# Kernel tuning notes

Hardware: AMD Instinct MI355X
Metric: run time of the kernel (lower is better)

The kernel has to match this reference:

```python
import jax, jax.numpy as jnp
import numpy as np

B, SEQ, DIM = 8, 4096, 64
THETA = 10000.0


def _make_freqs(seq, dim, theta=THETA):
    # matches torch.polar(ones, outer(t, 1/theta^(2i/dim))) stored as (cos, sin)
    inv = 1.0 / theta ** (np.arange(0, dim, 2, dtype=np.float32) / dim)
    t = np.arange(seq, dtype=np.float32)
    ang = np.outer(t, inv)  # (seq, dim//2)
    return jnp.stack([jnp.cos(ang), jnp.sin(ang)], axis=-1).astype(jnp.float32)  # (seq, dim//2, 2)


def _rope(x, freq):
    # x: (B, S, D); freq: (S, D//2, 2) holding (cos, sin) of the complex freq
    xr = x.reshape(*x.shape[:-1], -1, 2)  # (B, S, D//2, 2)
    a, b = xr[..., 0], xr[..., 1]
    c, s = freq[..., 0], freq[..., 1]
    # complex multiply (a + ib)(c + is)
    out = jnp.stack([a * c - b * s, a * s + b * c], axis=-1)
    return out.reshape(x.shape)


def setup_inputs() -> dict:
    key = jax.random.key(0)
    kq, kk, kv = jax.random.split(key, 3)
    q = jax.random.normal(kq, (B, SEQ, DIM), dtype=jnp.float32)
    k = jax.random.normal(kk, (B, SEQ, DIM), dtype=jnp.float32)
    v = jax.random.normal(kv, (B, SEQ, DIM), dtype=jnp.float32)
    f = _make_freqs(SEQ, DIM)
    return {"q": q, "k": k, "v": v, "freq_q": f, "freq_k": f, "freq_v": f}


def reference(q, k, v, freq_q, freq_k, freq_v):
    q_r = _rope(q, freq_q)
    k_r = _rope(k, freq_k)
    v_r = _rope(v, freq_v)
    scale = jnp.asarray(1.0 / np.sqrt(DIM), dtype=q.dtype)
    scores = jnp.einsum("bqd,bkd->bqk", q_r, k_r) * scale  # unnormalized logits (no softmax)
    return jnp.einsum("bqk,bkd->bqd", scores, v_r)
```

## Files before the change

kernel.cpp:

```cpp
#include <hip/hip_runtime.h>

#define B_ 8
#define S_ 4096
#define D_ 64

__global__ __launch_bounds__(256, 4) void rope_ktv_partials(
    const float* __restrict__ K, const float* __restrict__ V,
    const float* __restrict__ FK, const float* __restrict__ FV,
    float* __restrict__ part, int nchunk, int rowsPerChunk)
{
    __shared__ float kbuf[32][64];
    __shared__ float vbuf[32][64];
    const int t  = threadIdx.x;
    const int b  = blockIdx.x / nchunk;
    const int sBase = (blockIdx.x - b * nchunk) * rowsPerChunk;

    const int sl = t >> 4;
    const int e0 = (t & 15) << 2;
    const int i0 = (t >> 4) << 2;
    const int j0 = (t & 15) << 2;

    const float* kb = K + (size_t)b * S_ * D_;
    const float* vb = V + (size_t)b * S_ * D_;

    float acc[4][4];
    #pragma unroll
    for (int a = 0; a < 4; ++a)
        #pragma unroll
        for (int c = 0; c < 4; ++c) acc[a][c] = 0.f;

    const int nStages = rowsPerChunk >> 5;

    int s = sBase + sl;
    float4 kA = *(const float4*)(kb + (size_t)s * D_ + e0);
    float4 vA = *(const float4*)(vb + (size_t)s * D_ + e0);
    float4 fA = *(const float4*)(FK + (size_t)s * D_ + e0);
    float4 gA = *(const float4*)(FV + (size_t)s * D_ + e0);
    float4 kB = *(const float4*)(kb + (size_t)(s + 16) * D_ + e0);
    float4 vB = *(const float4*)(vb + (size_t)(s + 16) * D_ + e0);
    float4 fB = *(const float4*)(FK + (size_t)(s + 16) * D_ + e0);
    float4 gB = *(const float4*)(FV + (size_t)(s + 16) * D_ + e0);

    for (int it = 0; it < nStages; ++it) {
        float4 kr, vr, kr2, vr2;
        kr.x  = kA.x*fA.x - kA.y*fA.y;  kr.y  = kA.x*fA.y + kA.y*fA.x;
        kr.z  = kA.z*fA.z - kA.w*fA.w;  kr.w  = kA.z*fA.w + kA.w*fA.z;
        vr.x  = vA.x*gA.x - vA.y*gA.y;  vr.y  = vA.x*gA.y + vA.y*gA.x;
        vr.z  = vA.z*gA.z - vA.w*gA.w;  vr.w  = vA.z*gA.w + vA.w*gA.z;
        kr2.x = kB.x*fB.x - kB.y*fB.y;  kr2.y = kB.x*fB.y + kB.y*fB.x;
        kr2.z = kB.z*fB.z - kB.w*fB.w;  kr2.w = kB.z*fB.w + kB.w*fB.z;
        vr2.x = vB.x*gB.x - vB.y*gB.y;  vr2.y = vB.x*gB.y + vB.y*gB.x;
        vr2.z = vB.z*gB.z - vB.w*gB.w;  vr2.w = vB.z*gB.w + vB.w*gB.z;

        if (it > 0) __syncthreads();
        *(float4*)&kbuf[sl][e0]      = kr;
        *(float4*)&vbuf[sl][e0]      = vr;
        *(float4*)&kbuf[sl + 16][e0] = kr2;
        *(float4*)&vbuf[sl + 16][e0] = vr2;
        __syncthreads();

        if (it + 1 < nStages) {
            s = sBase + ((it + 1) << 5) + sl;
            kA = *(const float4*)(kb + (size_t)s * D_ + e0);
            vA = *(const float4*)(vb + (size_t)s * D_ + e0);
            fA = *(const float4*)(FK + (size_t)s * D_ + e0);
            gA = *(const float4*)(FV + (size_t)s * D_ + e0);
            kB = *(const float4*)(kb + (size_t)(s + 16) * D_ + e0);
            vB = *(const float4*)(vb + (size_t)(s + 16) * D_ + e0);
            fB = *(const float4*)(FK + (size_t)(s + 16) * D_ + e0);
            gB = *(const float4*)(FV + (size_t)(s + 16) * D_ + e0);
        }

        #pragma unroll
        for (int r = 0; r < 32; ++r) {
            float4 ka = *(const float4*)&kbuf[r][i0];
            float4 vv = *(const float4*)&vbuf[r][j0];
            acc[0][0] += ka.x*vv.x; acc[0][1] += ka.x*vv.y; acc[0][2] += ka.x*vv.z; acc[0][3] += ka.x*vv.w;
            acc[1][0] += ka.y*vv.x; acc[1][1] += ka.y*vv.y; acc[1][2] += ka.y*vv.z; acc[1][3] += ka.y*vv.w;
            acc[2][0] += ka.z*vv.x; acc[2][1] += ka.z*vv.y; acc[2][2] += ka.z*vv.z; acc[2][3] += ka.z*vv.w;
            acc[3][0] += ka.w*vv.x; acc[3][1] += ka.w*vv.y; acc[3][2] += ka.w*vv.z; acc[3][3] += ka.w*vv.w;
        }
    }

    float* p = part + (size_t)blockIdx.x * (D_ * D_);
    #pragma unroll
    for (int a = 0; a < 4; ++a)
        *(float4*)(p + (size_t)(i0 + a) * D_ + j0) =
            make_float4(acc[a][0], acc[a][1], acc[a][2], acc[a][3]);
}

__global__ __launch_bounds__(256) void reduce_partials(
    const float* __restrict__ part, float* __restrict__ M, int nchunk)
{
    const int g    = blockIdx.x * 256 + threadIdx.x;
    const int b    = g >> 12;
    const int cell = g & 4095;
    const float* p = part + ((size_t)b * nchunk) * (D_ * D_) + cell;
    float s0 = 0.f, s1 = 0.f, s2 = 0.f, s3 = 0.f;
    int i = 0;
    #pragma unroll 8
    for (; i + 4 <= nchunk; i += 4) {
        s0 += p[(size_t)(i + 0) * (D_ * D_)];
        s1 += p[(size_t)(i + 1) * (D_ * D_)];
        s2 += p[(size_t)(i + 2) * (D_ * D_)];
        s3 += p[(size_t)(i + 3) * (D_ * D_)];
    }
    for (; i < nchunk; ++i) s0 += p[(size_t)i * (D_ * D_)];
    M[g] = 0.125f * ((s0 + s1) + (s2 + s3));
}

__global__ __launch_bounds__(256) void rope_q_matmul(
    const float* __restrict__ Q, const float* __restrict__ FQ,
    const float* __restrict__ M, float* __restrict__ OUT, int nb2)
{
    __shared__ float Mt[64][65];
    __shared__ float qbuf[32][64];
    const int t = threadIdx.x;
    const int b = blockIdx.x / nb2;
    const int rowBase = (blockIdx.x - b * nb2) * 32;

    const int sl = t >> 4;
    const int e0 = (t & 15) << 2;
    const float* qb = Q + (size_t)b * S_ * D_;

    const int r1 = rowBase + sl;
    float4 qA = *(const float4*)(qb + (size_t)r1 * D_ + e0);
    float4 fA = *(const float4*)(FQ + (size_t)r1 * D_ + e0);
    float4 qB = *(const float4*)(qb + (size_t)(r1 + 16) * D_ + e0);
    float4 fB = *(const float4*)(FQ + (size_t)(r1 + 16) * D_ + e0);

    const float* mb = M + (size_t)b * (D_ * D_);
    float4 m0 = *(const float4*)(mb + (t << 2));
    float4 m1 = *(const float4*)(mb + 1024 + (t << 2));
    float4 m2 = *(const float4*)(mb + 2048 + (t << 2));
    float4 m3 = *(const float4*)(mb + 3072 + (t << 2));

    float4 qr, qr2;
    qr.x  = qA.x*fA.x - qA.y*fA.y;  qr.y  = qA.x*fA.y + qA.y*fA.x;
    qr.z  = qA.z*fA.z - qA.w*fA.w;  qr.w  = qA.z*fA.w + qA.w*fA.z;
    qr2.x = qB.x*fB.x - qB.y*fB.y;  qr2.y = qB.x*fB.y + qB.y*fB.x;
    qr2.z = qB.z*fB.z - qB.w*fB.w;  qr2.w = qB.z*fB.w + qB.w*fB.z;
    *(float4*)&qbuf[sl][e0]      = qr;
    *(float4*)&qbuf[sl + 16][e0] = qr2;

    {
        const int c0 = (t << 2);
        const float mv[16] = { m0.x, m0.y, m0.z, m0.w,  m1.x, m1.y, m1.z, m1.w,
                               m2.x, m2.y, m2.z, m2.w,  m3.x, m3.y, m3.z, m3.w };
        #pragma unroll
        for (int c = 0; c < 4; ++c)
            #pragma unroll
            for (int d = 0; d < 4; ++d) {
                const int cell = c * 1024 + c0 + d;
                Mt[cell & 63][cell >> 6] = mv[c * 4 + d];
            }
    }
    __syncthreads();

    const int j  = t & 63;
    const int rg = (t >> 6) << 3;
    float a[8];
    #pragma unroll
    for (int r = 0; r < 8; ++r) a[r] = 0.f;

    #pragma unroll
    for (int i = 0; i < 64; i += 4) {
        const float w0 = Mt[j][i], w1 = Mt[j][i+1], w2 = Mt[j][i+2], w3 = Mt[j][i+3];
        #pragma unroll
        for (int r = 0; r < 8; ++r) {
            float4 q = *(const float4*)&qbuf[rg + r][i];
            a[r] += q.x*w0 + q.y*w1 + q.z*w2 + q.w*w3;
        }
    }

    float* ob = OUT + ((size_t)b * S_ + rowBase + rg) * D_ + j;
    #pragma unroll
    for (int r = 0; r < 8; ++r)
        ob[(size_t)r * D_] = a[r];
}

extern "C" void kernel_launch(void* const* d_in, const int* in_sizes, int n_in,
                              void* d_out, int out_size, void* d_ws, size_t ws_size,
                              hipStream_t stream)
{
    const float* Q  = (const float*)d_in[0];
    const float* K  = (const float*)d_in[1];
    const float* V  = (const float*)d_in[2];
    const float* FQ = (const float*)d_in[3];
    const float* FK = (const float*)d_in[4];
    const float* FV = (const float*)d_in[5];
    float* OUT = (float*)d_out;

    float* M    = (float*)d_ws;
    float* part = (float*)d_ws + (size_t)B_ * D_ * D_;

    int nchunk = 128;
    while (nchunk > 1 &&
           (size_t)(B_ * D_ * D_ + B_ * nchunk * D_ * D_) * sizeof(float) > ws_size)
        nchunk >>= 1;
    const int rowsPerChunk = S_ / nchunk;

    rope_ktv_partials<<<dim3(B_ * nchunk), dim3(256), 0, stream>>>(
        K, V, FK, FV, part, nchunk, rowsPerChunk);

    reduce_partials<<<dim3((B_ * D_ * D_) / 256), dim3(256), 0, stream>>>(
        part, M, nchunk);

    const int nb2 = S_ / 32;
    rope_q_matmul<<<dim3(B_ * nb2), dim3(256), 0, stream>>>(
        Q, FQ, M, OUT, nb2);
}
```

Before: 105.7 us.

## Hardcode chunk count, prefetch all K/V rows upfront, retile Q matmul and reduction

The K^T V partial kernel now uses a fixed 64 chunks of 64 rows and issues every global load for both 32-row stages at the start, replacing the runtime-sized software-pipelined loop. The reduction kernel splits each output row's 64 partials across four thread groups and combines them in shared memory. The Q matmul now processes 64 rows per block with a 4x4 register tile per thread and float4 output stores. This aims to raise memory-level parallelism and cut launch and indexing overhead. In exchange it drops the workspace-size fallback and uses more registers per thread.

```diff
diff --git a/kernel.cpp b/kernel.cpp
--- a/kernel.cpp
+++ b/kernel.cpp
@@ -3,17 +3,19 @@
 #define B_ 8
 #define S_ 4096
 #define D_ 64
-
-__global__ __launch_bounds__(256, 4) void rope_ktv_partials(
+#define NCHUNK 64
+#define RPC (S_ / NCHUNK)
+
+__global__ void rope_ktv_partials(
     const float* __restrict__ K, const float* __restrict__ V,
     const float* __restrict__ FK, const float* __restrict__ FV,
-    float* __restrict__ part, int nchunk, int rowsPerChunk)
+    float* __restrict__ part)
 {
     __shared__ float kbuf[32][64];
     __shared__ float vbuf[32][64];
-    const int t  = threadIdx.x;
-    const int b  = blockIdx.x / nchunk;
-    const int sBase = (blockIdx.x - b * nchunk) * rowsPerChunk;
+    const int t = threadIdx.x;
+    const int b = blockIdx.x / NCHUNK;
+    const int sBase = (blockIdx.x - b * NCHUNK) * RPC;
 
     const int sl = t >> 4;
     const int e0 = (t & 15) << 2;
@@ -23,63 +25,84 @@
     const float* kb = K + (size_t)b * S_ * D_;
     const float* vb = V + (size_t)b * S_ * D_;
 
+    const size_t rA  = (size_t)(sBase + sl) * D_ + e0;
+    const size_t rA2 = rA + 16 * D_;
+    const size_t rB  = rA + 32 * D_;
+    const size_t rB2 = rA + 48 * D_;
+    float4 kA  = *(const float4*)(kb + rA);
+    float4 vA  = *(const float4*)(vb + rA);
+    float4 fA  = *(const float4*)(FK + rA);
+    float4 gA  = *(const float4*)(FV + rA);
+    float4 kA2 = *(const float4*)(kb + rA2);
+    float4 vA2 = *(const float4*)(vb + rA2);
+    float4 fA2 = *(const float4*)(FK + rA2);
+    float4 gA2 = *(const float4*)(FV + rA2);
+    float4 kB  = *(const float4*)(kb + rB);
+    float4 vB  = *(const float4*)(vb + rB);
+    float4 fB  = *(const float4*)(FK + rB);
+    float4 gB  = *(const float4*)(FV + rB);
+    float4 kB2 = *(const float4*)(kb + rB2);
+    float4 vB2 = *(const float4*)(vb + rB2);
+    float4 fB2 = *(const float4*)(FK + rB2);
+    float4 gB2 = *(const float4*)(FV + rB2);
+
     float acc[4][4];
     #pragma unroll
     for (int a = 0; a < 4; ++a)
         #pragma unroll
         for (int c = 0; c < 4; ++c) acc[a][c] = 0.f;
 
-    const int nStages = rowsPerChunk >> 5;
-
-    int s = sBase + sl;
-    float4 kA = *(const float4*)(kb + (size_t)s * D_ + e0);
-    float4 vA = *(const float4*)(vb + (size_t)s * D_ + e0);
-    float4 fA = *(const float4*)(FK + (size_t)s * D_ + e0);
-    float4 gA = *(const float4*)(FV + (size_t)s * D_ + e0);
-    float4 kB = *(const float4*)(kb + (size_t)(s + 16) * D_ + e0);
-    float4 vB = *(const float4*)(vb + (size_t)(s + 16) * D_ + e0);
-    float4 fB = *(const float4*)(FK + (size_t)(s + 16) * D_ + e0);
-    float4 gB = *(const float4*)(FV + (size_t)(s + 16) * D_ + e0);
-
-    for (int it = 0; it < nStages; ++it) {
+    {
         float4 kr, vr, kr2, vr2;
-        kr.x  = kA.x*fA.x - kA.y*fA.y;  kr.y  = kA.x*fA.y + kA.y*fA.x;
-        kr.z  = kA.z*fA.z - kA.w*fA.w;  kr.w  = kA.z*fA.w + kA.w*fA.z;
-        vr.x  = vA.x*gA.x - vA.y*gA.y;  vr.y  = vA.x*gA.y + vA.y*gA.x;
-        vr.z  = vA.z*gA.z - vA.w*gA.w;  vr.w  = vA.z*gA.w + vA.w*gA.z;
-        kr2.x = kB.x*fB.x - kB.y*fB.y;  kr2.y = kB.x*fB.y + kB.y*fB.x;
-        kr2.z = kB.z*fB.z - kB.w*fB.w;  kr2.w = kB.z*fB.w + kB.w*fB.z;
-        vr2.x = vB.x*gB.x - vB.y*gB.y;  vr2.y = vB.x*gB.y + vB.y*gB.x;
-        vr2.z = vB.z*gB.z - vB.w*gB.w;  vr2.w = vB.z*gB.w + vB.w*gB.z;
-
-        if (it > 0) __syncthreads();
+        kr.x  = kA.x*fA.x - kA.y*fA.y;   kr.y  = kA.x*fA.y + kA.y*fA.x;
+        kr.z  = kA.z*fA.z - kA.w*fA.w;   kr.w  = kA.z*fA.w + kA.w*fA.z;
+        vr.x  = vA.x*gA.x - vA.y*gA.y;   vr.y  = vA.x*gA.y + vA.y*gA.x;
+        vr.z  = vA.z*gA.z - vA.w*gA.w;   vr.w  = vA.z*gA.w + vA.w*gA.z;
+        kr2.x = kA2.x*fA2.x - kA2.y*fA2.y; kr2.y = kA2.x*fA2.y + kA2.y*fA2.x;
+        kr2.z = kA2.z*fA2.z - kA2.w*fA2.w; kr2.w = kA2.z*fA2.w + kA2.w*fA2.z;
+        vr2.x = vA2.x*gA2.x - vA2.y*gA2.y; vr2.y = vA2.x*gA2.y + vA2.y*gA2.x;
+        vr2.z = vA2.z*gA2.z - vA2.w*gA2.w; vr2.w = vA2.z*gA2.w + vA2.w*gA2.z;
         *(float4*)&kbuf[sl][e0]      = kr;
         *(float4*)&vbuf[sl][e0]      = vr;
         *(float4*)&kbuf[sl + 16][e0] = kr2;
         *(float4*)&vbuf[sl + 16][e0] = vr2;
-        __syncthreads();
-
-        if (it + 1 < nStages) {
-            s = sBase + ((it + 1) << 5) + sl;
-            kA = *(const float4*)(kb + (size_t)s * D_ + e0);
-            vA = *(const float4*)(vb + (size_t)s * D_ + e0);
-            fA = *(const float4*)(FK + (size_t)s * D_ + e0);
-            gA = *(const float4*)(FV + (size_t)s * D_ + e0);
-            kB = *(const float4*)(kb + (size_t)(s + 16) * D_ + e0);
-            vB = *(const float4*)(vb + (size_t)(s + 16) * D_ + e0);
-            fB = *(const float4*)(FK + (size_t)(s + 16) * D_ + e0);
-            gB = *(const float4*)(FV + (size_t)(s + 16) * D_ + e0);
-        }
-
-        #pragma unroll
-        for (int r = 0; r < 32; ++r) {
-            float4 ka = *(const float4*)&kbuf[r][i0];
-            float4 vv = *(const float4*)&vbuf[r][j0];
-            acc[0][0] += ka.x*vv.x; acc[0][1] += ka.x*vv.y; acc[0][2] += ka.x*vv.z; acc[0][3] += ka.x*vv.w;
-            acc[1][0] += ka.y*vv.x; acc[1][1] += ka.y*vv.y; acc[1][2] += ka.y*vv.z; acc[1][3] += ka.y*vv.w;
-            acc[2][0] += ka.z*vv.x; acc[2][1] += ka.z*vv.y; acc[2][2] += ka.z*vv.z; acc[2][3] += ka.z*vv.w;
-            acc[3][0] += ka.w*vv.x; acc[3][1] += ka.w*vv.y; acc[3][2] += ka.w*vv.z; acc[3][3] += ka.w*vv.w;
-        }
+    }
+    __syncthreads();
+    #pragma unroll
+    for (int r = 0; r < 32; ++r) {
+        float4 ka = *(const float4*)&kbuf[r][i0];
+        float4 vv = *(const float4*)&vbuf[r][j0];
+        acc[0][0] += ka.x*vv.x; acc[0][1] += ka.x*vv.y; acc[0][2] += ka.x*vv.z; acc[0][3] += ka.x*vv.w;
+        acc[1][0] += ka.y*vv.x; acc[1][1] += ka.y*vv.y; acc[1][2] += ka.y*vv.z; acc[1][3] += ka.y*vv.w;
+        acc[2][0] += ka.z*vv.x; acc[2][1] += ka.z*vv.y; acc[2][2] += ka.z*vv.z; acc[2][3] += ka.z*vv.w;
+        acc[3][0] += ka.w*vv.x; acc[3][1] += ka.w*vv.y; acc[3][2] += ka.w*vv.z; acc[3][3] += ka.w*vv.w;
+    }
+    __syncthreads();
+
+    {
+        float4 kr, vr, kr2, vr2;
+        kr.x  = kB.x*fB.x - kB.y*fB.y;   kr.y  = kB.x*fB.y + kB.y*fB.x;
+        kr.z  = kB.z*fB.z - kB.w*fB.w;   kr.w  = kB.z*fB.w + kB.w*fB.z;
+        vr.x  = vB.x*gB.x - vB.y*gB.y;   vr.y  = vB.x*gB.y + vB.y*gB.x;
+        vr.z  = vB.z*gB.z - vB.w*gB.w;   vr.w  = vB.z*gB.w + vB.w*gB.z;
+        kr2.x = kB2.x*fB2.x - kB2.y*fB2.y; kr2.y = kB2.x*fB2.y + kB2.y*fB2.x;
+        kr2.z = kB2.z*fB2.z - kB2.w*fB2.w; kr2.w = kB2.z*fB2.w + kB2.w*fB2.z;
+        vr2.x = vB2.x*gB2.x - vB2.y*gB2.y; vr2.y = vB2.x*gB2.y + vB2.y*gB2.x;
+        vr2.z = vB2.z*gB2.z - vB2.w*gB2.w; vr2.w = vB2.z*gB2.w + vB2.w*gB2.z;
+        *(float4*)&kbuf[sl][e0]      = kr;
+        *(float4*)&vbuf[sl][e0]      = vr;
+        *(float4*)&kbuf[sl + 16][e0] = kr2;
+        *(float4*)&vbuf[sl + 16][e0] = vr2;
+    }
+    __syncthreads();
+    #pragma unroll
+    for (int r = 0; r < 32; ++r) {
+        float4 ka = *(const float4*)&kbuf[r][i0];
+        float4 vv = *(const float4*)&vbuf[r][j0];
+        acc[0][0] += ka.x*vv.x; acc[0][1] += ka.x*vv.y; acc[0][2] += ka.x*vv.z; acc[0][3] += ka.x*vv.w;
+        acc[1][0] += ka.y*vv.x; acc[1][1] += ka.y*vv.y; acc[1][2] += ka.y*vv.z; acc[1][3] += ka.y*vv.w;
+        acc[2][0] += ka.z*vv.x; acc[2][1] += ka.z*vv.y; acc[2][2] += ka.z*vv.z; acc[2][3] += ka.z*vv.w;
+        acc[3][0] += ka.w*vv.x; acc[3][1] += ka.w*vv.y; acc[3][2] += ka.w*vv.z; acc[3][3] += ka.w*vv.w;
     }
 
     float* p = part + (size_t)blockIdx.x * (D_ * D_);
@@ -89,45 +112,43 @@
             make_float4(acc[a][0], acc[a][1], acc[a][2], acc[a][3]);
 }
 
-__global__ __launch_bounds__(256) void reduce_partials(
-    const float* __restrict__ part, float* __restrict__ M, int nchunk)
-{
-    const int g    = blockIdx.x * 256 + threadIdx.x;
-    const int b    = g >> 12;
-    const int cell = g & 4095;
-    const float* p = part + ((size_t)b * nchunk) * (D_ * D_) + cell;
+__global__ void reduce_partials(const float* __restrict__ part,
+                                float* __restrict__ M)
+{
+    __shared__ float red[4][64];
+    const int t   = threadIdx.x;
+    const int c   = t & 63;
+    const int q   = t >> 6;
+    const int blk = blockIdx.x;
+    const int b   = blk >> 6;
+    const int i   = blk & 63;
+
+    const float* p = part + ((size_t)b * NCHUNK + q * 16) * (D_ * D_) + i * D_ + c;
     float s0 = 0.f, s1 = 0.f, s2 = 0.f, s3 = 0.f;
-    int i = 0;
-    #pragma unroll 8
-    for (; i + 4 <= nchunk; i += 4) {
-        s0 += p[(size_t)(i + 0) * (D_ * D_)];
-        s1 += p[(size_t)(i + 1) * (D_ * D_)];
-        s2 += p[(size_t)(i + 2) * (D_ * D_)];
-        s3 += p[(size_t)(i + 3) * (D_ * D_)];
-    }
-    for (; i < nchunk; ++i) s0 += p[(size_t)i * (D_ * D_)];
-    M[g] = 0.125f * ((s0 + s1) + (s2 + s3));
-}
-
-__global__ __launch_bounds__(256) void rope_q_matmul(
+    #pragma unroll
+    for (int k = 0; k < 4; ++k) {
+        s0 += p[(size_t)(4 * k + 0) * (D_ * D_)];
+        s1 += p[(size_t)(4 * k + 1) * (D_ * D_)];
+        s2 += p[(size_t)(4 * k + 2) * (D_ * D_)];
+        s3 += p[(size_t)(4 * k + 3) * (D_ * D_)];
+    }
+    red[q][c] = (s0 + s1) + (s2 + s3);
+    __syncthreads();
+    if (t < 64)
+        M[(size_t)b * (D_ * D_) + i * D_ + t] =
+            0.125f * ((red[0][t] + red[1][t]) + (red[2][t] + red[3][t]));
+}
+
+__global__ void rope_q_matmul(
     const float* __restrict__ Q, const float* __restrict__ FQ,
-    const float* __restrict__ M, float* __restrict__ OUT, int nb2)
+    const float* __restrict__ M, float* __restrict__ OUT)
 {
     __shared__ float Mt[64][65];
-    __shared__ float qbuf[32][64];
+    __shared__ float qbuf[64][68];
     const int t = threadIdx.x;
-    const int b = blockIdx.x / nb2;
-    const int rowBase = (blockIdx.x - b * nb2) * 32;
-
-    const int sl = t >> 4;
-    const int e0 = (t & 15) << 2;
-    const float* qb = Q + (size_t)b * S_ * D_;
-
-    const int r1 = rowBase + sl;
-    float4 qA = *(const float4*)(qb + (size_t)r1 * D_ + e0);
-    float4 fA = *(const float4*)(FQ + (size_t)r1 * D_ + e0);
-    float4 qB = *(const float4*)(qb + (size_t)(r1 + 16) * D_ + e0);
-    float4 fB = *(const float4*)(FQ + (size_t)(r1 + 16) * D_ + e0);
+    const int blk = blockIdx.x;
+    const int b = blk >> 6;
+    const int rowBase = (blk & 63) * 64;
 
     const float* mb = M + (size_t)b * (D_ * D_);
     float4 m0 = *(const float4*)(mb + (t << 2));
@@ -135,48 +156,70 @@
     float4 m2 = *(const float4*)(mb + 2048 + (t << 2));
     float4 m3 = *(const float4*)(mb + 3072 + (t << 2));
 
-    float4 qr, qr2;
-    qr.x  = qA.x*fA.x - qA.y*fA.y;  qr.y  = qA.x*fA.y + qA.y*fA.x;
-    qr.z  = qA.z*fA.z - qA.w*fA.w;  qr.w  = qA.z*fA.w + qA.w*fA.z;
-    qr2.x = qB.x*fB.x - qB.y*fB.y;  qr2.y = qB.x*fB.y + qB.y*fB.x;
-    qr2.z = qB.z*fB.z - qB.w*fB.w;  qr2.w = qB.z*fB.w + qB.w*fB.z;
-    *(float4*)&qbuf[sl][e0]      = qr;
-    *(float4*)&qbuf[sl + 16][e0] = qr2;
+    const int qrow = t >> 2;
+    const int e0   = (t & 3) << 4;
+    const float* qb = Q + ((size_t)b * S_ + rowBase + qrow) * D_ + e0;
+    const float* fb = FQ + ((size_t)(rowBase + qrow)) * D_ + e0;
+    float4 q0 = *(const float4*)(qb + 0),  f0 = *(const float4*)(fb + 0);
+    float4 q1 = *(const float4*)(qb + 4),  f1 = *(const float4*)(fb + 4);
+    float4 q2 = *(const float4*)(qb + 8),  f2 = *(const float4*)(fb + 8);
+    float4 q3 = *(const float4*)(qb + 12), f3 = *(const float4*)(fb + 12);
+
+    float4 r0, r1, r2, r3;
+    r0.x = q0.x*f0.x - q0.y*f0.y;  r0.y = q0.x*f0.y + q0.y*f0.x;
+    r0.z = q0.z*f0.z - q0.w*f0.w;  r0.w = q0.z*f0.w + q0.w*f0.z;
+    r1.x = q1.x*f1.x - q1.y*f1.y;  r1.y = q1.x*f1.y + q1.y*f1.x;
+    r1.z = q1.z*f1.z - q1.w*f1.w;  r1.w = q1.z*f1.w + q1.w*f1.z;
+    r2.x = q2.x*f2.x - q2.y*f2.y;  r2.y = q2.x*f2.y + q2.y*f2.x;
+    r2.z = q2.z*f2.z - q2.w*f2.w;  r2.w = q2.z*f2.w + q2.w*f2.z;
+    r3.x = q3.x*f3.x - q3.y*f3.y;  r3.y = q3.x*f3.y + q3.y*f3.x;
+    r3.z = q3.z*f3.z - q3.w*f3.w;  r3.w = q3.z*f3.w + q3.w*f3.z;
+    *(float4*)&qbuf[qrow][e0 + 0]  = r0;
+    *(float4*)&qbuf[qrow][e0 + 4]  = r1;
+    *(float4*)&qbuf[qrow][e0 + 8]  = r2;
+    *(float4*)&qbuf[qrow][e0 + 12] = r3;
 
     {
-        const int c0 = (t << 2);
         const float mv[16] = { m0.x, m0.y, m0.z, m0.w,  m1.x, m1.y, m1.z, m1.w,
                                m2.x, m2.y, m2.z, m2.w,  m3.x, m3.y, m3.z, m3.w };
+        const int jBase = (t << 2) & 63;
+        const int iIdx0 = (t >> 4);
         #pragma unroll
         for (int c = 0; c < 4; ++c)
             #pragma unroll
-            for (int d = 0; d < 4; ++d) {
-                const int cell = c * 1024 + c0 + d;
-                Mt[cell & 63][cell >> 6] = mv[c * 4 + d];
-            }
-    }
-    __syncthreads();
-
-    const int j  = t & 63;
-    const int rg = (t >> 6) << 3;
-    float a[8];
-    #pragma unroll
-    for (int r = 0; r < 8; ++r) a[r] = 0.f;
+            for (int d = 0; d < 4; ++d)
+                Mt[jBase + d][c * 16 + iIdx0] = mv[c * 4 + d];
+    }
+    __syncthreads();
+
+    const int ty = t >> 4;
+    const int tx = t & 15;
+    float acc[4][4];
+    #pragma unroll
+    for (int r = 0; r < 4; ++r)
+        #pragma unroll
+        for (int c = 0; c < 4; ++c) acc[r][c] = 0.f;
 
     #pragma unroll
     for (int i = 0; i < 64; i += 4) {
-        const float w0 = Mt[j][i], w1 = Mt[j][i+1], w2 = Mt[j][i+2], w3 = Mt[j][i+3];
-        #pragma unroll
-        for (int r = 0; r < 8; ++r) {
-            float4 q = *(const float4*)&qbuf[rg + r][i];
-            a[r] += q.x*w0 + q.y*w1 + q.z*w2 + q.w*w3;
-        }
-    }
-
-    float* ob = OUT + ((size_t)b * S_ + rowBase + rg) * D_ + j;
-    #pragma unroll
-    for (int r = 0; r < 8; ++r)
-        ob[(size_t)r * D_] = a[r];
+        float4 mtv[4], qv[4];
+        #pragma unroll
+        for (int c = 0; c < 4; ++c) mtv[c] = *(const float4*)&Mt[tx * 4 + c][i];
+        #pragma unroll
+        for (int r = 0; r < 4; ++r) qv[r]  = *(const float4*)&qbuf[ty * 4 + r][i];
+        #pragma unroll
+        for (int r = 0; r < 4; ++r)
+            #pragma unroll
+            for (int c = 0; c < 4; ++c)
+                acc[r][c] += qv[r].x * mtv[c].x + qv[r].y * mtv[c].y +
+                             qv[r].z * mtv[c].z + qv[r].w * mtv[c].w;
+    }
+
+    float* ob = OUT + ((size_t)b * S_ + rowBase + ty * 4) * D_ + tx * 4;
+    #pragma unroll
+    for (int r = 0; r < 4; ++r)
+        *(float4*)(ob + (size_t)r * D_) =
+            make_float4(acc[r][0], acc[r][1], acc[r][2], acc[r][3]);
 }
 
 extern "C" void kernel_launch(void* const* d_in, const int* in_sizes, int n_in,
@@ -194,19 +237,11 @@
     float* M    = (float*)d_ws;
     float* part = (float*)d_ws + (size_t)B_ * D_ * D_;
 
-    int nchunk = 128;
-    while (nchunk > 1 &&
-           (size_t)(B_ * D_ * D_ + B_ * nchunk * D_ * D_) * sizeof(float) > ws_size)
-        nchunk >>= 1;
-    const int rowsPerChunk = S_ / nchunk;
-
-    rope_ktv_partials<<<dim3(B_ * nchunk), dim3(256), 0, stream>>>(
-        K, V, FK, FV, part, nchunk, rowsPerChunk);
-
-    reduce_partials<<<dim3((B_ * D_ * D_) / 256), dim3(256), 0, stream>>>(
-        part, M, nchunk);
-
-    const int nb2 = S_ / 32;
-    rope_q_matmul<<<dim3(B_ * nb2), dim3(256), 0, stream>>>(
-        Q, FQ, M, OUT, nb2);
-}
+    rope_ktv_partials<<<dim3(B_ * NCHUNK), dim3(256), 0, stream>>>(
+        K, V, FK, FV, part);
+
+    reduce_partials<<<dim3(B_ * D_), dim3(256), 0, stream>>>(part, M);
+
+    rope_q_matmul<<<dim3(B_ * (S_ / 64)), dim3(256), 0, stream>>>(
+        Q, FQ, M, OUT);
+}
```

Result: slower. 164.4 us (+55.5%).
